# Kernel optimization log

Hardware: AMD Instinct MI355X
Metric: run time of the kernel (lower is better)

## Reference

```python
import jax, jax.numpy as jnp
import numpy as np

PRE_NMS_THRESH = 0.05
PRE_NMS_TOP_N = 1000
NMS_THRESH = 0.6
FPN_POST_NMS_TOP_N = 100
MIN_SIZE = 0.0
STRIDE = 8
NEG = -1e9  # padding score for invalid slots (avoids inf/nan in grads)


def setup_inputs() -> dict:
    key = jax.random.key(0)
    k1, k2, k3 = jax.random.split(key, 3)
    N, H, W = 16, 400, 608
    # stride-8 FCOS location grid, xy order
    xs = (jnp.arange(W, dtype=jnp.float32) * STRIDE) + STRIDE // 2
    ys = (jnp.arange(H, dtype=jnp.float32) * STRIDE) + STRIDE // 2
    gy, gx = jnp.meshgrid(ys, xs, indexing='ij')
    locations = jnp.stack([gx.reshape(-1), gy.reshape(-1)], axis=1)  # [H*W, 2]
    box_cls = jax.random.normal(k1, (N, 1, H, W), dtype=jnp.float32)
    box_regression = jax.random.uniform(k2, (N, 4, H, W), dtype=jnp.float32) * 64.0
    centerness = jax.random.normal(k3, (N, 1, H, W), dtype=jnp.float32)
    image_sizes = jnp.tile(jnp.array([[H * STRIDE, W * STRIDE]], dtype=jnp.int32), (N, 1))  # (h, w)
    return {"locations": locations, "box_cls": box_cls,
            "box_regression": box_regression, "centerness": centerness,
            "image_sizes": image_sizes}


def _nms_one(boxes, scores):
    """Greedy NMS over K fixed slots. boxes [K,4], scores [K] (NEG = invalid)."""
    order = jnp.argsort(-scores)
    b = boxes[order]
    s = scores[order]
    area = (b[:, 2] - b[:, 0]) * (b[:, 3] - b[:, 1])
    lt = jnp.maximum(b[:, None, :2], b[None, :, :2])   # [K,K,2]
    rb = jnp.minimum(b[:, None, 2:], b[None, :, 2:])
    wh = jnp.clip(rb - lt, 0.0)
    inter = wh[..., 0] * wh[..., 1]
    iou = inter / (area[:, None] + area[None, :] - inter + 1e-9)
    K = b.shape[0]
    ar = jnp.arange(K)

    def body(keep, i):
        kept_i = keep[i] & (s[i] > NEG / 2)
        keep = keep & ~(kept_i & (iou[i] > NMS_THRESH) & (ar > i))
        return keep, kept_i

    _, kept = jax.lax.scan(body, jnp.ones((K,), dtype=bool), ar)
    s_out = jnp.where(kept & (s > NEG / 2), s, NEG)
    return b, s_out


def reference(locations, box_cls, box_regression, centerness, image_sizes):
    N, C, H, W = box_cls.shape
    # [N,C,H,W] -> [N,H*W,C] ; BINARY, num_classes=2 -> C=1
    scores = jax.nn.sigmoid(box_cls.transpose(0, 2, 3, 1).reshape(N, -1))  # [N,HW]
    reg = box_regression.transpose(0, 2, 3, 1).reshape(N, -1, 4)           # [N,HW,4]
    ctr = jax.nn.sigmoid(centerness.transpose(0, 2, 3, 1).reshape(N, -1))  # [N,HW]
    cand = scores > PRE_NMS_THRESH           # candidate mask from raw cls score
    s = scores * ctr                         # score used for ranking
    sm = jnp.where(cand, s, NEG)
    vals, idx = jax.lax.top_k(sm, PRE_NMS_TOP_N)                 # [N,K]
    valid = jnp.take_along_axis(cand, idx, axis=1)               # [N,K]
    g_reg = jnp.take_along_axis(reg, idx[..., None], axis=1)     # [N,K,4]
    g_loc = locations[idx]                                       # [N,K,2]
    x1 = g_loc[..., 0] - g_reg[..., 0]
    y1 = g_loc[..., 1] - g_reg[..., 1]
    x2 = g_loc[..., 0] + g_reg[..., 2]
    y2 = g_loc[..., 1] + g_reg[..., 3]
    hw = image_sizes.astype(jnp.float32)
    wmax = hw[:, 1:2] - 1.0
    hmax = hw[:, 0:1] - 1.0
    x1 = jnp.clip(x1, 0.0, wmax); x2 = jnp.clip(x2, 0.0, wmax)
    y1 = jnp.clip(y1, 0.0, hmax); y2 = jnp.clip(y2, 0.0, hmax)
    keep_size = ((x2 - x1 + 1.0) >= MIN_SIZE) & ((y2 - y1 + 1.0) >= MIN_SIZE)
    valid = valid & keep_size
    boxes = jnp.stack([x1, y1, x2, y2], axis=-1)                 # [N,K,4]
    sc = jnp.where(valid, vals, NEG)
    b_sorted, s_nms = jax.vmap(_nms_one)(boxes, sc)              # [N,K,4],[N,K]
    fv, fi = jax.lax.top_k(s_nms, FPN_POST_NMS_TOP_N)            # [N,100]
    fb = jnp.take_along_axis(b_sorted, fi[..., None], axis=1)    # [N,100,4]
    fvalid = fv > NEG / 2
    fb = jnp.where(fvalid[..., None], fb, 0.0)
    fs = jnp.where(fvalid, fv, 0.0)
    labels = jnp.where(fvalid, 1, 0).astype(jnp.int32)
    dets = jnp.concatenate([fb, fs[..., None]], axis=-1)         # [N,100,5]
    return dets, labels, fvalid
```

## Files before the change

kernel.cpp:

```cpp
#include <hip/hip_runtime.h>
#include <cstdint>


#define NIMG 16
#define WW 608
#define HW 243200
#define NF4 60800
#define TOPK 1000
#define NBINS 512
#define NB2 2048
#define SCAN_BLOCKS 60
#define SCAN_THREADS 256
#define F4_PER_BLOCK 1024
#define LS 128
#define PCAP 1024
#define MCAP 2048
#define EDS_CAP 512
#define NEGV (-1e9f)

__device__ __forceinline__ float sigm(float x) { return 1.0f / (1.0f + expf(-x)); }

__device__ __forceinline__ int binof(float v) {
  if (!(v > 0.0f)) return 0;
  int b = (int)(v * (float)NBINS);
  return b > (NBINS - 1) ? (NBINS - 1) : b;
}

__device__ __forceinline__ int bucketof(float v) {
  if (!(v > 0.0f)) return 0;
  int b = (int)(v * (float)NB2);
  return b > (NB2 - 1) ? (NB2 - 1) : b;
}

__device__ __forceinline__ void find_thresh_bin(const unsigned* h, const unsigned* chunk,
                                                unsigned T, unsigned* outbs, int tid) {
  unsigned v = (tid < 32) ? chunk[tid] : 0u;
  unsigned inc = v;
#pragma unroll
  for (int d = 1; d < 32; d <<= 1) {
    unsigned o = __shfl_down(inc, d, 64);
    if (tid + d < 32) inc += o;
  }
  unsigned long long m = __ballot((tid < 32) && (inc >= T));
  if (m == 0ull) { if (tid == 0) *outbs = 0u; return; }
  int cc = 63 - __clzll(m);
  unsigned above = __shfl(inc, cc) - chunk[cc];
  unsigned v2 = (tid < 16) ? h[cc * 16 + tid] : 0u;
  unsigned inc2 = v2;
#pragma unroll
  for (int d = 1; d < 16; d <<= 1) {
    unsigned o = __shfl_down(inc2, d, 64);
    if (tid + d < 16) inc2 += o;
  }
  unsigned long long m2 = __ballot((tid < 16) && (above + inc2 >= T));
  int bb = (m2 != 0ull) ? (63 - __clzll(m2)) : 0;
  if (tid == 0) *outbs = (unsigned)(cc * 16 + bb);
}

__global__ __launch_bounds__(SCAN_THREADS) void k_scanstore(
    const float4* __restrict__ cls, const float4* __restrict__ ctr,
    const float* __restrict__ reg, const int* __restrict__ isz,
    float* __restrict__ preval, unsigned* __restrict__ pregi,
    float4* __restrict__ prebox, unsigned* __restrict__ pcnt) {
  __shared__ unsigned lh[NBINS];
  __shared__ float lval[PCAP];
  __shared__ unsigned lgi[PCAP];
  __shared__ unsigned chunk[NBINS / 16];
  __shared__ unsigned sLb, pcl;
  const int tid = threadIdx.x;
  for (int b = tid; b < NBINS; b += SCAN_THREADS) lh[b] = 0u;
  if (tid == 0) pcl = 0u;
  __syncthreads();
  const int n = blockIdx.y;
  const float4* c4 = cls + (size_t)n * NF4;
  const float4* t4 = ctr + (size_t)n * NF4;
  const int base = blockIdx.x * F4_PER_BLOCK;
  float4 cv[4], tv[4];
  float smr[16];
  bool ok[4];
#pragma unroll
  for (int e = 0; e < 4; ++e) {
    int i = base + e * SCAN_THREADS + tid;
    ok[e] = (i < NF4);
    if (ok[e]) { cv[e] = c4[i]; tv[e] = t4[i]; }
  }
#pragma unroll
  for (int e = 0; e < 4; ++e) {
    const float* cc = (const float*)&cv[e];
    const float* tt = (const float*)&tv[e];
#pragma unroll
    for (int k = 0; k < 4; ++k) {
      float sm = NEGV;
      if (ok[e]) {
        float sc = sigm(cc[k]);
        sm = (sc > 0.05f) ? sc * sigm(tt[k]) : NEGV;
        atomicAdd(&lh[binof(sm)], 1u);
      }
      smr[e * 4 + k] = sm;
    }
  }
  __syncthreads();
  if (tid < NBINS / 16) {
    unsigned s = 0;
    for (int k = 0; k < 16; ++k) s += lh[tid * 16 + k];
    chunk[tid] = s;
  }
  __syncthreads();
  if (tid < 64) find_thresh_bin(lh, chunk, LS, &sLb, tid);
  __syncthreads();
  const unsigned Lb = sLb;
#pragma unroll
  for (int e = 0; e < 4; ++e) {
    if (ok[e]) {
#pragma unroll
      for (int k = 0; k < 4; ++k) {
        float sm = smr[e * 4 + k];
        if ((unsigned)binof(sm) >= Lb) {
          unsigned gi = (unsigned)((base + e * SCAN_THREADS + tid) * 4 + k);
          unsigned p = atomicAdd(&pcl, 1u);
          if (p < PCAP) { lval[p] = sm; lgi[p] = gi; }
        }
      }
    }
  }
  __syncthreads();
  const int bslot = n * SCAN_BLOCKS + blockIdx.x;
  unsigned m = pcl; if (m > PCAP) m = PCAP;
  const float wmax = (float)(isz[n * 2 + 1] - 1);
  const float hmax = (float)(isz[n * 2 + 0] - 1);
  const float* rg = reg + (size_t)n * 4 * HW;
  const size_t gbase = (size_t)bslot * PCAP;
  for (unsigned k = tid; k < m; k += SCAN_THREADS) {
    unsigned gi = lgi[k];
    float val = lval[k];
    int wx = (int)gi % WW, hy = (int)gi / WW;
    float lx = (float)(wx * 8 + 4), ly = (float)(hy * 8 + 4);
    float l = rg[0 * HW + gi], tt = rg[1 * HW + gi];
    float rr = rg[2 * HW + gi], bb = rg[3 * HW + gi];
    float x1 = lx - l, y1 = ly - tt, x2 = lx + rr, y2 = ly + bb;
    x1 = fminf(fmaxf(x1, 0.0f), wmax);
    x2 = fminf(fmaxf(x2, 0.0f), wmax);
    y1 = fminf(fmaxf(y1, 0.0f), hmax);
    y2 = fminf(fmaxf(y2, 0.0f), hmax);
    bool valid = (((x2 - x1 + 1.0f) >= 0.0f) && ((y2 - y1 + 1.0f) >= 0.0f));
    float4 bx = valid ? make_float4(x1, y1, x2, y2)
                      : make_float4(-1.f, -1.f, -1.f, -1.f);
    preval[gbase + k] = val;
    pregi[gbase + k] = gi;
    prebox[gbase + k] = bx;
  }
  if (tid == 0) pcnt[bslot] = m;
}

__global__ __launch_bounds__(1024) void k_fcr_nms(
    const float* __restrict__ preval, const unsigned* __restrict__ pregi,
    const float4* __restrict__ prebox, const unsigned* __restrict__ pcnt,
    const int* __restrict__ isz, float* __restrict__ out) {
  __shared__ __align__(16) unsigned long long smemA[2816];
  __shared__ __align__(16) unsigned long long sk[MCAP];
  __shared__ __align__(16) float4 skbox[MCAP];
  __shared__ unsigned bh[NB2];
  __shared__ unsigned bbase[NB2];
  __shared__ unsigned chunk[32];
  __shared__ unsigned offs[SCAN_BLOCKS + 1];
  __shared__ unsigned wsum[16];
  __shared__ unsigned sB2, mc, ecl;
  const int n = blockIdx.x;
  const int tid = threadIdx.x;
  const int wid = tid >> 6, lane = tid & 63;

  for (int b = tid; b < NB2; b += 1024) bh[b] = 0u;
  if (tid < 64) {
    int l = tid;
    int v = (l < SCAN_BLOCKS) ? (int)pcnt[n * SCAN_BLOCKS + l] : 0;
    int inc = v;
#pragma unroll
    for (int d = 1; d < 64; d <<= 1) {
      int o = __shfl_up(inc, d, 64);
      if (l >= d) inc += o;
    }
    if (l < SCAN_BLOCKS) offs[l + 1] = (unsigned)inc;
    if (l == 0) offs[0] = 0u;
  }
  __syncthreads();
  const unsigned P = offs[SCAN_BLOCKS];
  const size_t ibase = (size_t)n * SCAN_BLOCKS * PCAP;
  for (unsigned p = tid; p < P; p += 1024) {
    int lo = 0, hi = SCAN_BLOCKS - 1;
    while (lo < hi) {
      int mid = (lo + hi + 1) >> 1;
      if (offs[mid] <= p) lo = mid; else hi = mid - 1;
    }
    float v = preval[ibase + (size_t)lo * PCAP + (p - offs[lo])];
    atomicAdd(&bh[bucketof(v)], 1u);
  }
  __syncthreads();
  if (tid < 32) {
    unsigned s = 0;
    const int b0 = tid * 64;
    for (int k = 0; k < 64; ++k) s += bh[b0 + k];
    chunk[tid] = s;
  }
  __syncthreads();
  if (tid < 64) {
    unsigned v = (tid < 32) ? chunk[tid] : 0u;
    unsigned inc = v;
#pragma unroll
    for (int d = 1; d < 32; d <<= 1) {
      unsigned o = __shfl_down(inc, d, 64);
      if (tid + d < 32) inc += o;
    }
    unsigned long long m = __ballot((tid < 32) && (inc >= TOPK));
    int cc = (m != 0ull) ? (63 - __clzll(m)) : 0;
    unsigned above = (m != 0ull) ? (__shfl(inc, cc) - chunk[cc]) : 0u;
    unsigned inc2 = bh[cc * 64 + tid];
#pragma unroll
    for (int d = 1; d < 64; d <<= 1) {
      unsigned o = __shfl_down(inc2, d, 64);
      if (tid + d < 64) inc2 += o;
    }
    unsigned long long m2 = __ballot(above + inc2 >= TOPK);
    int bb = (m2 != 0ull) ? (63 - __clzll(m2)) : 0;
    if (tid == 0) sB2 = (m != 0ull) ? (unsigned)(cc * 64 + bb) : 0u;
  }
  __syncthreads();
  const unsigned B2 = sB2;
  {
    int g0 = tid * 2, g1 = g0 + 1;
    unsigned a0 = bh[NB2 - 1 - g0];
    unsigned a1 = bh[NB2 - 1 - g1];
    unsigned pair = a0 + a1;
    unsigned inc = pair;
#pragma unroll
    for (int d = 1; d < 64; d <<= 1) {
      unsigned o = __shfl_up(inc, d, 64);
      if (lane >= d) inc += o;
    }
    if (lane == 63) wsum[wid] = inc;
    __syncthreads();
    if (tid < 64) {
      unsigned v = (tid < 16) ? wsum[tid] : 0u;
      unsigned i2 = v;
#pragma unroll
      for (int d = 1; d < 16; d <<= 1) {
        unsigned o = __shfl_up(i2, d, 64);
        if (tid >= d) i2 += o;
      }
      if (tid < 16) wsum[tid] = i2 - v;
    }
    __syncthreads();
    unsigned excl = inc - pair + wsum[wid];
    bbase[NB2 - 1 - g0] = excl;
    bbase[NB2 - 1 - g1] = excl + a0;
  }
  __syncthreads();
  if (tid == 0) {
    unsigned mm = bbase[B2] + bh[B2];
    mc = (mm > MCAP) ? MCAP : mm;
  }
  for (int b = tid; b < NB2; b += 1024) bh[b] = 0u;
  __syncthreads();
  const unsigned M = mc;
  for (unsigned p = tid; p < P; p += 1024) {
    int lo = 0, hi = SCAN_BLOCKS - 1;
    while (lo < hi) {
      int mid = (lo + hi + 1) >> 1;
      if (offs[mid] <= p) lo = mid; else hi = mid - 1;
    }
    size_t idx = ibase + (size_t)lo * PCAP + (p - offs[lo]);
    float v = preval[idx];
    int b = bucketof(v);
    if ((unsigned)b >= B2) {
      unsigned gi = pregi[idx];
      unsigned pos = bbase[b] + atomicAdd(&bh[b], 1u);
      if (pos < MCAP) {
        sk[pos] = ((unsigned long long)__float_as_uint(v) << 32) |
                  (unsigned long long)(~gi);
        skbox[pos] = prebox[idx];
      }
    }
  }
  float4* sb = (float4*)smemA;
  float* ssc = (float*)((char*)smemA + 16384);
  unsigned char* kept = (unsigned char*)((char*)smemA + 20480);
  int* sel = (int*)((char*)smemA + 21600);
  if (tid < TOPK) { sb[tid] = make_float4(0.f, 0.f, 0.f, 0.f); ssc[tid] = NEGV; }
  __syncthreads();
  for (unsigned s = tid; s < M; s += 1024) {
    const unsigned long long mykey = sk[s];
    const float val = __uint_as_float((unsigned)(mykey >> 32));
    int b = bucketof(val);
    unsigned beg = bbase[b];
    unsigned end = (b > 0) ? bbase[b - 1] : M;
    if (end > M) end = M;
    unsigned rank = beg;
    for (unsigned t = beg; t < end; ++t) rank += (sk[t] > mykey) ? 1u : 0u;
    if (rank >= TOPK) continue;
    float4 bx = skbox[s];
    sb[rank] = bx;
    ssc[rank] = (bx.x < 0.0f) ? NEGV : val;
  }
  __syncthreads();
  unsigned* ccount = bh;
  unsigned* cidx = bh + 1024;
  unsigned* cbase = bbase;
  unsigned* eds = bbase + 1024;
  unsigned* eds2 = bbase + 1536;
  const int W = isz[n * 2 + 1], H = isz[n * 2 + 0];
  int cw = (W + 31) >> 5; if (cw < 128) cw = 128;
  int ch = (H + 31) >> 5; if (ch < 128) ch = 128;
  const int cols = (W + cw - 1) / cw;
  const int rows = (H + ch - 1) / ch;
  const float icw = 1.0f / (float)cw, ich = 1.0f / (float)ch;
  ccount[tid] = 0u;
  if (tid == 0) ecl = 0u;
  __syncthreads();
  int mycell = -1;
  if (tid < TOPK && ssc[tid] > NEGV * 0.5f) {
    float4 b = sb[tid];
    int cx = (int)((b.x + b.z) * 0.5f * icw);
    int cy = (int)((b.y + b.w) * 0.5f * ich);
    cx = cx < 0 ? 0 : (cx > cols - 1 ? cols - 1 : cx);
    cy = cy < 0 ? 0 : (cy > rows - 1 ? rows - 1 : cy);
    mycell = cy * cols + cx;
    atomicAdd(&ccount[mycell], 1u);
  }
  __syncthreads();
  {
    unsigned v = ccount[tid];
    unsigned inc = v;
#pragma unroll
    for (int d = 1; d < 64; d <<= 1) {
      unsigned o = __shfl_up(inc, d, 64);
      if (lane >= d) inc += o;
    }
    if (lane == 63) wsum[wid] = inc;
    __syncthreads();
    if (tid < 64) {
      unsigned vv = (tid < 16) ? wsum[tid] : 0u;
      unsigned i2 = vv;
#pragma unroll
      for (int d = 1; d < 16; d <<= 1) {
        unsigned o = __shfl_up(i2, d, 64);
        if (tid >= d) i2 += o;
      }
      if (tid < 16) wsum[tid] = i2 - vv;
    }
    __syncthreads();
    cbase[tid] = inc - v + wsum[wid];
  }
  __syncthreads();
  ccount[tid] = 0u;
  __syncthreads();
  if (mycell >= 0) {
    unsigned pos = cbase[mycell] + atomicAdd(&ccount[mycell], 1u);
    cidx[pos] = (unsigned)tid;
  }
  __syncthreads();
  if (mycell >= 0) {
    const int j = tid;
    float4 bj = sb[j];
    float aj = (bj.z - bj.x) * (bj.w - bj.y);
    int cx = mycell % cols, cy = mycell / cols;
    int x0 = cx > 0 ? cx - 1 : 0, x1c = cx < cols - 1 ? cx + 1 : cols - 1;
    int y0 = cy > 0 ? cy - 1 : 0, y1c = cy < rows - 1 ? cy + 1 : rows - 1;
    for (int yy = y0; yy <= y1c; ++yy) {
      for (int xx = x0; xx <= x1c; ++xx) {
        unsigned c = (unsigned)(yy * cols + xx);
        unsigned b0 = cbase[c], cnt = ccount[c];
        for (unsigned k2 = 0; k2 < cnt; ++k2) {
          unsigned i = cidx[b0 + k2];
          if (i >= (unsigned)j) continue;
          float4 bi = sb[i];
          float ai = (bi.z - bi.x) * (bi.w - bi.y);
          float ltx = fmaxf(bi.x, bj.x), lty = fmaxf(bi.y, bj.y);
          float rbx = fminf(bi.z, bj.z), rby = fminf(bi.w, bj.w);
          float wv = fmaxf(rbx - ltx, 0.0f), hv = fmaxf(rby - lty, 0.0f);
          float inter = wv * hv;
          float iou = inter / (ai + aj - inter + 1e-9f);
          if (iou > 0.6f) {
            unsigned p2 = atomicAdd(&ecl, 1u);
            if (p2 < EDS_CAP) eds[p2] = (i << 10) | (unsigned)j;
          }
        }
      }
    }
  }
  __syncthreads();
  unsigned E = ecl; if (E > EDS_CAP) E = EDS_CAP;
  for (int k = tid; k < TOPK; k += 1024) kept[k] = 1;
  __syncthreads();
  for (int e = tid; e < (int)E; e += 1024) {
    unsigned v = eds[e];
    unsigned r = 0;
    for (unsigned t = 0; t < E; ++t) r += (eds[t] < v) ? 1u : 0u;
    eds2[r] = v;
  }
  __syncthreads();
  if (tid == 0) {
    for (int e = 0; e < (int)E; ++e) {
      unsigned i2 = eds2[e] >> 10, j2 = eds2[e] & 1023u;
      if (kept[i2]) kept[j2] = 0;
    }
  }
  __syncthreads();
  if (tid < 100) sel[tid] = -1;
  __syncthreads();
  if (tid < 64) {
    int c0 = tid * 16;
    int c1 = c0 + 16; if (c1 > TOPK) c1 = TOPK;
    int cnt = 0;
    for (int e = c0; e < c1; ++e)
      if (kept[e] && ssc[e] > NEGV * 0.5f) cnt++;
    int inc = cnt;
#pragma unroll
    for (int d = 1; d < 64; d <<= 1) {
      int o = __shfl_up(inc, d, 64);
      if (tid >= d) inc += o;
    }
    unsigned r = (unsigned)(inc - cnt);
    for (int e = c0; e < c1; ++e) {
      if (kept[e] && ssc[e] > NEGV * 0.5f) {
        if (r < 100u) sel[r] = e;
        r++;
      }
    }
  }
  __syncthreads();
  for (int k = tid; k < 100; k += 1024) {
    int s = sel[k];
    float x1 = 0.f, y1 = 0.f, x2 = 0.f, y2 = 0.f, sc = 0.f, lab = 0.f, fv = 0.f;
    if (s >= 0) {
      float4 b = sb[s];
      x1 = b.x; y1 = b.y; x2 = b.z; y2 = b.w;
      sc = ssc[s]; lab = 1.0f; fv = 1.0f;
    }
    int o = (n * 100 + k) * 5;
    out[o + 0] = x1; out[o + 1] = y1; out[o + 2] = x2; out[o + 3] = y2; out[o + 4] = sc;
    out[NIMG * 500 + n * 100 + k] = lab;
    out[NIMG * 600 + n * 100 + k] = fv;
  }
}

extern "C" void kernel_launch(void* const* d_in, const int* in_sizes, int n_in,
                              void* d_out, int out_size, void* d_ws, size_t ws_size,
                              hipStream_t stream) {
  const float4* cls4 = (const float4*)d_in[1];
  const float* reg = (const float*)d_in[2];
  const float4* ctr4 = (const float4*)d_in[3];
  const int* isz = (const int*)d_in[4];
  float* out = (float*)d_out;
  uint8_t* w = (uint8_t*)d_ws;

  const size_t NSLOT = (size_t)NIMG * SCAN_BLOCKS * PCAP;
  uint8_t* p = w;
  float* preval = (float*)p;      p += NSLOT * 4;
  unsigned* pregi = (unsigned*)p; p += NSLOT * 4;
  float4* prebox = (float4*)p;    p += NSLOT * 16;
  unsigned* pcnt = (unsigned*)p;  p += (size_t)NIMG * SCAN_BLOCKS * 4;
  (void)ws_size;

  dim3 g1(SCAN_BLOCKS, NIMG);
  k_scanstore<<<g1, SCAN_THREADS, 0, stream>>>(cls4, ctr4, reg, isz,
                                               preval, pregi, prebox, pcnt);
  k_fcr_nms<<<NIMG, 1024, 0, stream>>>(preval, pregi, prebox, pcnt, isz, out);
}
```

Baseline: 56.78 us.

## Stage compacted candidate scores in LDS and shrink per-block candidate capacity

New measurement: 50.27 us. 1.13x faster.

```diff
diff --git a/kernel.cpp b/kernel.cpp
--- a/kernel.cpp
+++ b/kernel.cpp
@@ -12,8 +12,9 @@
 #define SCAN_BLOCKS 60
 #define SCAN_THREADS 256
 #define F4_PER_BLOCK 1024
-#define LS 128
-#define PCAP 1024
+#define LS 64
+#define PCAP 256
+#define PLDS 6144
 #define MCAP 2048
 #define EDS_CAP 512
 #define NEGV (-1e9f)
@@ -159,6 +160,7 @@
   __shared__ __align__(16) unsigned long long smemA[2816];
   __shared__ __align__(16) unsigned long long sk[MCAP];
   __shared__ __align__(16) float4 skbox[MCAP];
+  __shared__ __align__(16) unsigned long long pls[PLDS];
   __shared__ unsigned bh[NB2];
   __shared__ unsigned bbase[NB2];
   __shared__ unsigned chunk[32];
@@ -185,7 +187,23 @@
   __syncthreads();
   const unsigned P = offs[SCAN_BLOCKS];
   const size_t ibase = (size_t)n * SCAN_BLOCKS * PCAP;
-  for (unsigned p = tid; p < P; p += 1024) {
+  for (int idx = tid; idx < SCAN_BLOCKS * PCAP; idx += 1024) {
+    int s = idx / PCAP, k = idx % PCAP;
+    unsigned c = offs[s + 1] - offs[s];
+    if ((unsigned)k < c) {
+      unsigned dst = offs[s] + (unsigned)k;
+      if (dst < PLDS) {
+        float v = preval[ibase + idx];
+        pls[dst] = ((unsigned long long)__float_as_uint(v) << 32) |
+                   (unsigned long long)(unsigned)idx;
+      }
+    }
+  }
+  __syncthreads();
+  const unsigned PS = (P < PLDS) ? P : PLDS;
+  for (unsigned p = tid; p < PS; p += 1024)
+    atomicAdd(&bh[bucketof(__uint_as_float((unsigned)(pls[p] >> 32)))], 1u);
+  for (unsigned p = PLDS + (unsigned)tid; p < P; p += 1024) {
     int lo = 0, hi = SCAN_BLOCKS - 1;
     while (lo < hi) {
       int mid = (lo + hi + 1) >> 1;
@@ -261,7 +279,22 @@
   for (int b = tid; b < NB2; b += 1024) bh[b] = 0u;
   __syncthreads();
   const unsigned M = mc;
-  for (unsigned p = tid; p < P; p += 1024) {
+  for (unsigned p = tid; p < PS; p += 1024) {
+    unsigned long long e = pls[p];
+    float v = __uint_as_float((unsigned)(e >> 32));
+    int b = bucketof(v);
+    if ((unsigned)b >= B2) {
+      unsigned idx = (unsigned)(e & 0xFFFFFFFFull);
+      unsigned gi = pregi[ibase + idx];
+      unsigned pos = bbase[b] + atomicAdd(&bh[b], 1u);
+      if (pos < MCAP) {
+        sk[pos] = ((unsigned long long)__float_as_uint(v) << 32) |
+                  (unsigned long long)(~gi);
+        skbox[pos] = prebox[ibase + idx];
+      }
+    }
+  }
+  for (unsigned p = PLDS + (unsigned)tid; p < P; p += 1024) {
     int lo = 0, hi = SCAN_BLOCKS - 1;
     while (lo < hi) {
       int mid = (lo + hi + 1) >> 1;
```
